# Kernel tuning notes

Measured on AMD Instinct MI355X. Metric: run time of the kernel, lower is better.

Reference implementation:

```python
import jax, jax.numpy as jnp
import numpy as np

N_NODES = 50000
EPS = 1e-5


def sage_conv_max(x, src, dst, W_l, b_l, W_r):
    # PyG SAGEConv(aggr='max'): out = lin_l(max_j x_j) + lin_r(x_i)
    msg = x[src]                                   # [E, d] gather
    agg = jnp.full((x.shape[0], x.shape[1]), -jnp.inf, dtype=x.dtype)
    agg = agg.at[dst].max(msg)                     # scatter-max over edges
    agg = jnp.where(jnp.isneginf(agg), 0.0, agg)   # isolated nodes -> 0 (PyG convention)
    return agg @ W_l.T + b_l + x @ W_r.T


def batch_norm(x, gamma, beta):
    mean = jnp.mean(x, axis=0)
    var = jnp.var(x, axis=0)
    return (x - mean) * jax.lax.rsqrt(var + EPS) * gamma + beta


def setup_inputs() -> dict:
    key = jax.random.key(0)
    ks = jax.random.split(key, 10)
    d_in, d_h, d_out = 128, 128, 32
    s = lambda fan: 1.0 / np.sqrt(fan)
    return {
        "x": jax.random.normal(ks[0], (N_NODES, d_in), dtype=jnp.float32),
        "edge_index": jax.random.randint(ks[1], (2, 800000), 0, N_NODES, dtype=jnp.int32),
        "W_l1": jax.random.uniform(ks[2], (d_h, d_in), jnp.float32, -s(d_in), s(d_in)),
        "b_l1": jnp.zeros((d_h,), jnp.float32),
        "W_r1": jax.random.uniform(ks[3], (d_h, d_in), jnp.float32, -s(d_in), s(d_in)),
        "gamma1": jnp.ones((d_h,), jnp.float32),
        "beta1": jnp.zeros((d_h,), jnp.float32),
        "W_l2": jax.random.uniform(ks[4], (d_out, d_h), jnp.float32, -s(d_h), s(d_h)),
        "b_l2": jnp.zeros((d_out,), jnp.float32),
        "W_r2": jax.random.uniform(ks[5], (d_out, d_h), jnp.float32, -s(d_h), s(d_h)),
    }


def reference(x, edge_index, W_l1, b_l1, W_r1, gamma1, beta1, W_l2, b_l2, W_r2):
    src, dst = edge_index[0], edge_index[1]
    h = sage_conv_max(x, src, dst, W_l1, b_l1, W_r1)
    h = batch_norm(h, gamma1, beta1)
    h = jax.nn.relu(h)
    # dropout is identity at inference
    return sage_conv_max(h, src, dst, W_l2, b_l2, W_r2)
```

## Files before the change

### kernel.cpp

```cpp
#include <hip/hip_runtime.h>
#include <math.h>
#include <float.h>

#define N_NODES 50000
#define N_EDGES 800000
#define NB 392
#define EB 2048
#define NBUCK 196
#define BSH 8
#define CAP 36
#define SEGC 4864
#define CELLS_PER_BUCKET (NB * CAP)
#define FBLK 782

typedef __attribute__((ext_vector_type(8))) short bf16x8;
typedef __attribute__((ext_vector_type(4))) float f32x4;

static __device__ __forceinline__ unsigned short f2bf(float f) {
  unsigned int u = __float_as_uint(f);
  u = (u + 0x7fff + ((u >> 16) & 1)) >> 16;
  return (unsigned short)u;
}

__global__ __launch_bounds__(256) void setup_kernel(
    const int* __restrict__ src, const int* __restrict__ dst,
    unsigned int* __restrict__ pairs, int* __restrict__ counts,
    const float* __restrict__ x, const float* __restrict__ Wl1,
    const float* __restrict__ Wr1, const float* __restrict__ Wl2,
    const float* __restrict__ Wr2, unsigned int* __restrict__ x_bf,
    unsigned short* __restrict__ Wcat1, unsigned short* __restrict__ Wcat2,
    float* __restrict__ gsums) {
  const int b = blockIdx.x, tid = threadIdx.x;
  if (b < NB) {
    __shared__ int cur[NBUCK];
    if (tid < NBUCK) cur[tid] = 0;
    __syncthreads();
#pragma unroll
    for (int it = 0; it < EB / 256; ++it) {
      int e = b * EB + it * 256 + tid;
      if (e < N_EDGES) {
        int d = dst[e];
        int bk = d >> BSH;
        int p = atomicAdd(&cur[bk], 1);
        if (p < CAP)
          pairs[(size_t)(bk * NB + b) * CAP + p] =
              (unsigned)src[e] | ((unsigned)(d & 255) << 16);
      }
    }
    __syncthreads();
    if (tid < NBUCK) {
      int c = cur[tid];
      counts[tid * NB + b] = c > CAP ? CAP : c;
    }
  } else if (b < NB + 6250) {
    int i = (b - NB) * 256 + tid;
    float4 v = ((const float4*)x)[i];
    uint2 o;
    o.x = (unsigned int)f2bf(v.x) | ((unsigned int)f2bf(v.y) << 16);
    o.y = (unsigned int)f2bf(v.z) | ((unsigned int)f2bf(v.w) << 16);
    ((uint2*)x_bf)[i] = o;
  } else if (b < NB + 6410) {
    int i = (b - NB - 6250) * 256 + tid;
    if (i < 32768) {
      int n = i >> 8, k = i & 255;
      float w = (k < 128) ? Wl1[n * 128 + k] : Wr1[n * 128 + (k - 128)];
      Wcat1[i] = f2bf(w);
    } else if (i < 40960) {
      int j = i - 32768;
      int n = j >> 8, k = j & 255;
      float w = (k < 128) ? Wl2[n * 128 + k] : Wr2[n * 128 + (k - 128)];
      Wcat2[j] = f2bf(w);
    }
  } else {
#pragma unroll
    for (int i = 0; i < 8; ++i) gsums[i * 256 + tid] = 0.f;
  }
}

__global__ __launch_bounds__(1024) void bucket_sort(const unsigned int* __restrict__ pairs,
                                                    const int* __restrict__ counts,
                                                    unsigned int* __restrict__ rowinfo,
                                                    int* __restrict__ elist) {
  __shared__ int hist[256], cpos[256], cnt[NB];
  __shared__ int wsum[4];
  const int b = blockIdx.x, tid = threadIdx.x;
  const size_t s0 = (size_t)b * CELLS_PER_BUCKET;
  if (tid < 256) hist[tid] = 0;
  if (tid < NB) cnt[tid] = counts[b * NB + tid];
  __syncthreads();
  for (int p = tid; p < CELLS_PER_BUCKET; p += 1024) {
    int c = p / CAP, s = p - c * CAP;
    if (s < cnt[c]) {
      unsigned int pr = pairs[s0 + p];
      atomicAdd(&hist[(pr >> 16) & 255], 1);
    }
  }
  __syncthreads();
  int incl = 0, h = 0;
  if (tid < 256) {
    const int l = tid & 63;
    h = hist[tid];
    incl = h;
#pragma unroll
    for (int off = 1; off < 64; off <<= 1) {
      int t = __shfl_up(incl, off, 64);
      if (l >= off) incl += t;
    }
    if (l == 63) wsum[tid >> 6] = incl;
  }
  __syncthreads();
  if (tid < 64) {
    int v = (tid < 4) ? wsum[tid] : 0;
#pragma unroll
    for (int off = 1; off < 4; off <<= 1) {
      int t = __shfl_up(v, off, 64);
      if (tid >= off) v += t;
    }
    if (tid < 4) wsum[tid] = v;
  }
  __syncthreads();
  if (tid < 256) {
    const int w = tid >> 6;
    int tot = incl + ((w > 0) ? wsum[w - 1] : 0);
    int excl = tot - h;
    cpos[tid] = excl;
    int node = (b << BSH) + tid;
    if (node < N_NODES)
      rowinfo[node] = (unsigned)(b * SEGC + excl) | ((unsigned)h << 20);
  }
  __syncthreads();
  for (int p = tid; p < CELLS_PER_BUCKET; p += 1024) {
    int c = p / CAP, s = p - c * CAP;
    if (s < cnt[c]) {
      unsigned int pr = pairs[s0 + p];
      int loc = atomicAdd(&cpos[(pr >> 16) & 255], 1);
      elist[b * SEGC + loc] = (int)(pr & 0xffffu);
    }
  }
}

#define ASTR 264

template <int NCOLT, int LDO, bool BF16OUT, bool STATS, bool BN>
__global__ __launch_bounds__(256) void fused_layer(
    const uint4* __restrict__ feat4,
    const unsigned short* __restrict__ Ab,
    const unsigned int* __restrict__ rowinfo,
    const int* __restrict__ elist,
    const unsigned short* __restrict__ Wcat, const float* __restrict__ bias,
    unsigned short* __restrict__ outb, float* __restrict__ outf,
    float* __restrict__ gsums, const float* __restrict__ gamma,
    const float* __restrict__ beta, int N) {
  __shared__ unsigned short Alds[64 * ASTR];
  __shared__ float s_sum[128], s_sq[128];
  __shared__ float s_scale[128], s_shift[128];
  const int tid = threadIdx.x;
  const int rowBase = blockIdx.x * 64;

  if (STATS && tid < 128) { s_sum[tid] = 0.f; s_sq[tid] = 0.f; }
  if (BN) {
    if (tid < 128) {
      float sm = 0.f, sq = 0.f;
#pragma unroll
      for (int r = 0; r < 8; ++r) {
        sm += gsums[r * 256 + tid];
        sq += gsums[r * 256 + 128 + tid];
      }
      const float inv = 1.f / (float)N_NODES;
      float mean = sm * inv;
      float var = sq * inv - mean * mean;
      float sc = gamma[tid] * rsqrtf(var + 1e-5f);
      s_scale[tid] = sc;
      s_shift[tid] = beta[tid] - mean * sc;
    }
    __syncthreads();
  }

#pragma unroll
  for (int it = 0; it < 4; ++it) {
    int f = tid + it * 256;
    int r = f >> 4, seg = f & 15;
    int n = rowBase + r;
    if (n >= N) n = N - 1;
    int4 d = *(const int4*)(Ab + (size_t)n * 128 + seg * 8);
    if (BN) {
      int kb = seg * 8;
      unsigned int* dp = (unsigned int*)&d;
#pragma unroll
      for (int c = 0; c < 4; ++c) {
        int k0 = kb + 2 * c;
        float lo = __uint_as_float(dp[c] << 16);
        float hi = __uint_as_float(dp[c] & 0xffff0000u);
        lo = fmaxf(lo * s_scale[k0] + s_shift[k0], 0.f);
        hi = fmaxf(hi * s_scale[k0 + 1] + s_shift[k0 + 1], 0.f);
        dp[c] = (unsigned)f2bf(lo) | ((unsigned)f2bf(hi) << 16);
      }
    }
    *(int4*)(&Alds[r * ASTR + 128 + seg * 8]) = d;
  }

  const int wv = tid >> 6;
  const int lane = tid & 63;
  const int eslot = lane >> 4;
  const int fq = lane & 15;
  for (int it = 0; it < 16; ++it) {
    int r = wv * 16 + it;
    int node = rowBase + r;
    if (node >= N) node = N - 1;
    unsigned int info = rowinfo[node];
    int e0 = (int)(info & 0xFFFFFu);
    int deg = (int)(info >> 20);
    int e1 = e0 + deg;
    float m[8];
#pragma unroll
    for (int j = 0; j < 8; ++j) m[j] = -FLT_MAX;
    if (deg > 0) {
      const int last = e1 - 1;
      for (int base = e0; base < e1; base += 16) {
        int idx[4];
#pragma unroll
        for (int q = 0; q < 4; ++q) {
          int e = base + q * 4 + eslot;
          if (e > last) e = last;
          idx[q] = elist[e];
        }
        uint4 v[4];
#pragma unroll
        for (int q = 0; q < 4; ++q) v[q] = feat4[(size_t)idx[q] * 16 + fq];
#pragma unroll
        for (int q = 0; q < 4; ++q) {
          const unsigned int* pv = (const unsigned int*)&v[q];
#pragma unroll
          for (int c = 0; c < 4; ++c) {
            m[2 * c]     = fmaxf(m[2 * c],     __uint_as_float(pv[c] << 16));
            m[2 * c + 1] = fmaxf(m[2 * c + 1], __uint_as_float(pv[c] & 0xffff0000u));
          }
        }
      }
    }
#pragma unroll
    for (int j = 0; j < 8; ++j) {
      m[j] = fmaxf(m[j], __shfl_xor(m[j], 16, 64));
      m[j] = fmaxf(m[j], __shfl_xor(m[j], 32, 64));
    }
    if (eslot == 0) {
      if (deg == 0) {
#pragma unroll
        for (int j = 0; j < 8; ++j) m[j] = 0.f;
      } else if (BN) {
#pragma unroll
        for (int j = 0; j < 8; ++j) {
          int col = fq * 8 + j;
          m[j] = fmaxf(m[j] * s_scale[col] + s_shift[col], 0.f);
        }
      }
      int4 o;
      unsigned int* op = (unsigned int*)&o;
      op[0] = (unsigned)f2bf(m[0]) | ((unsigned)f2bf(m[1]) << 16);
      op[1] = (unsigned)f2bf(m[2]) | ((unsigned)f2bf(m[3]) << 16);
      op[2] = (unsigned)f2bf(m[4]) | ((unsigned)f2bf(m[5]) << 16);
      op[3] = (unsigned)f2bf(m[6]) | ((unsigned)f2bf(m[7]) << 16);
      *(int4*)(&Alds[r * ASTR + fq * 8]) = o;
    }
  }

  const int ln15 = lane & 15;
  const int quad = lane >> 4;
  const int ct0 = (NCOLT == 8) ? wv * 2 : 0;
  bf16x8 breg[8][2];
#pragma unroll
  for (int ks = 0; ks < 8; ++ks) {
    const int off = ks * 32 + quad * 8;
#pragma unroll
    for (int j = 0; j < 2; ++j)
      breg[ks][j] = *(const bf16x8*)(Wcat + (size_t)((ct0 + j) * 16 + ln15) * 256 + off);
  }
  __syncthreads();

  float psum[2] = {0.f, 0.f}, psq[2] = {0.f, 0.f};
  const int S0 = (NCOLT == 8) ? 0 : wv;
  const int SN = (NCOLT == 8) ? 4 : 1;
#pragma unroll
  for (int si = 0; si < 4; ++si) {
    if (si >= SN) break;
    const int s = S0 + si;
    const int mrow = s * 16;
    bf16x8 a[8];
#pragma unroll
    for (int ks = 0; ks < 8; ++ks)
      a[ks] = *(const bf16x8*)(&Alds[(mrow + ln15) * ASTR + ks * 32 + quad * 8]);
    f32x4 acc[2] = {};
#pragma unroll
    for (int ks = 0; ks < 8; ++ks)
#pragma unroll
      for (int j = 0; j < 2; ++j)
        acc[j] = __builtin_amdgcn_mfma_f32_16x16x32_bf16(a[ks], breg[ks][j], acc[j], 0, 0, 0);
#pragma unroll
    for (int j = 0; j < 2; ++j) {
      int col = (ct0 + j) * 16 + ln15;
      float bv = bias[col];
#pragma unroll
      for (int i = 0; i < 4; ++i) {
        int r = rowBase + mrow + quad * 4 + i;
        if (r < N) {
          float val = acc[j][i] + bv;
          if (STATS) { psum[j] += val; psq[j] += val * val; }
          if (BF16OUT)
            outb[(size_t)r * LDO + col] = f2bf(val);
          else
            outf[(size_t)r * LDO + col] = val;
        }
      }
    }
  }

  if (STATS) {
#pragma unroll
    for (int j = 0; j < 2; ++j) {
      int col = (ct0 + j) * 16 + ln15;
      atomicAdd(&s_sum[col], psum[j]);
      atomicAdd(&s_sq[col], psq[j]);
    }
    __syncthreads();
    if (tid < 128) {
      int rep = blockIdx.x & 7;
      atomicAdd(&gsums[rep * 256 + tid], s_sum[tid]);
      atomicAdd(&gsums[rep * 256 + 128 + tid], s_sq[tid]);
    }
  }
}

extern "C" void kernel_launch(void* const* d_in, const int* in_sizes, int n_in,
                              void* d_out, int out_size, void* d_ws, size_t ws_size,
                              hipStream_t stream) {
  (void)in_sizes; (void)n_in; (void)out_size; (void)ws_size;
  const float* x     = (const float*)d_in[0];
  const int*   eidx  = (const int*)d_in[1];
  const float* W_l1  = (const float*)d_in[2];
  const float* b_l1  = (const float*)d_in[3];
  const float* W_r1  = (const float*)d_in[4];
  const float* gamma = (const float*)d_in[5];
  const float* beta  = (const float*)d_in[6];
  const float* W_l2  = (const float*)d_in[7];
  const float* b_l2  = (const float*)d_in[8];
  const float* W_r2  = (const float*)d_in[9];
  const int* srcp = eidx;
  const int* dstp = eidx + N_EDGES;
  float* out = (float*)d_out;

  int* wsi = (int*)d_ws;
  float* gsums   = (float*)wsi;
  unsigned int* rowinfo = (unsigned int*)(wsi + 2048);
  int*   counts  = wsi + 52224;
  int*   elist   = wsi + 129056;
  unsigned int* pairs   = (unsigned int*)(wsi + 1082400);
  unsigned int* x_bf    = (unsigned int*)(wsi + 3848352);
  unsigned int* h_bf    = (unsigned int*)(wsi + 10248352);
  unsigned short* Wcat1 = (unsigned short*)(wsi + 13448352);
  unsigned short* Wcat2 = (unsigned short*)(wsi + 13464736);

  setup_kernel<<<dim3(NB + 6410 + 1), 256, 0, stream>>>(
      srcp, dstp, pairs, counts, x, W_l1, W_r1, W_l2, W_r2, x_bf, Wcat1, Wcat2, gsums);

  bucket_sort<<<dim3(NBUCK), 1024, 0, stream>>>(pairs, counts, rowinfo, elist);

  fused_layer<8, 128, true, true, false><<<dim3(FBLK), 256, 0, stream>>>(
      (const uint4*)x_bf, (const unsigned short*)x_bf, rowinfo, elist, Wcat1, b_l1,
      (unsigned short*)h_bf, nullptr, gsums, nullptr, nullptr, N_NODES);

  fused_layer<2, 32, false, false, true><<<dim3(FBLK), 256, 0, stream>>>(
      (const uint4*)h_bf, (const unsigned short*)h_bf, rowinfo, elist, Wcat2, b_l2,
      nullptr, out, gsums, gamma, beta, N_NODES);
}
```

Baseline: 213.9 us.

## Split x bf16 conversion and weight packing across setup and sort kernels

The x-to-bf16 conversion is split in half. The first half stays in the edge-binning kernel, and the second half, the weight concatenation and the gsums zeroing move into extra blocks of the bucket-sort kernel. The bucket sort launches only 196 large blocks and otherwise leaves much of the GPU idle, so the intent is to balance the two launches by filling that idle capacity with independent conversion work. Adding non-sort blocks to the 1024-thread sort kernel could delay scheduling of the sort blocks or raise resource contention.

```diff
diff --git a/kernel.cpp b/kernel.cpp
--- a/kernel.cpp
+++ b/kernel.cpp
@@ -12,6 +12,9 @@
 #define SEGC 4864
 #define CELLS_PER_BUCKET (NB * CAP)
 #define FBLK 782
+#define XH1_BLKS 3125
+#define XH2_BLKS 782
+#define WC_BLKS 40
 
 typedef __attribute__((ext_vector_type(8))) short bf16x8;
 typedef __attribute__((ext_vector_type(4))) float f32x4;
@@ -22,14 +25,10 @@
   return (unsigned short)u;
 }
 
-__global__ __launch_bounds__(256) void setup_kernel(
+__global__ __launch_bounds__(256) void setup_a(
     const int* __restrict__ src, const int* __restrict__ dst,
     unsigned int* __restrict__ pairs, int* __restrict__ counts,
-    const float* __restrict__ x, const float* __restrict__ Wl1,
-    const float* __restrict__ Wr1, const float* __restrict__ Wl2,
-    const float* __restrict__ Wr2, unsigned int* __restrict__ x_bf,
-    unsigned short* __restrict__ Wcat1, unsigned short* __restrict__ Wcat2,
-    float* __restrict__ gsums) {
+    const float* __restrict__ x, unsigned int* __restrict__ x_bf) {
   const int b = blockIdx.x, tid = threadIdx.x;
   if (b < NB) {
     __shared__ int cur[NBUCK];
@@ -52,38 +51,56 @@
       int c = cur[tid];
       counts[tid * NB + b] = c > CAP ? CAP : c;
     }
-  } else if (b < NB + 6250) {
+  } else {
     int i = (b - NB) * 256 + tid;
     float4 v = ((const float4*)x)[i];
     uint2 o;
     o.x = (unsigned int)f2bf(v.x) | ((unsigned int)f2bf(v.y) << 16);
     o.y = (unsigned int)f2bf(v.z) | ((unsigned int)f2bf(v.w) << 16);
     ((uint2*)x_bf)[i] = o;
-  } else if (b < NB + 6410) {
-    int i = (b - NB - 6250) * 256 + tid;
-    if (i < 32768) {
-      int n = i >> 8, k = i & 255;
-      float w = (k < 128) ? Wl1[n * 128 + k] : Wr1[n * 128 + (k - 128)];
-      Wcat1[i] = f2bf(w);
-    } else if (i < 40960) {
-      int j = i - 32768;
-      int n = j >> 8, k = j & 255;
-      float w = (k < 128) ? Wl2[n * 128 + k] : Wr2[n * 128 + (k - 128)];
-      Wcat2[j] = f2bf(w);
-    }
-  } else {
-#pragma unroll
-    for (int i = 0; i < 8; ++i) gsums[i * 256 + tid] = 0.f;
-  }
-}
-
-__global__ __launch_bounds__(1024) void bucket_sort(const unsigned int* __restrict__ pairs,
-                                                    const int* __restrict__ counts,
-                                                    unsigned int* __restrict__ rowinfo,
-                                                    int* __restrict__ elist) {
+  }
+}
+
+__global__ __launch_bounds__(1024) void sort_b(
+    const unsigned int* __restrict__ pairs, const int* __restrict__ counts,
+    unsigned int* __restrict__ rowinfo, int* __restrict__ elist,
+    const float* __restrict__ x, const float* __restrict__ Wl1,
+    const float* __restrict__ Wr1, const float* __restrict__ Wl2,
+    const float* __restrict__ Wr2, unsigned int* __restrict__ x_bf,
+    unsigned short* __restrict__ Wcat1, unsigned short* __restrict__ Wcat2,
+    float* __restrict__ gsums) {
+  const int b = blockIdx.x, tid = threadIdx.x;
+  if (b >= NBUCK) {
+    int bb = b - NBUCK;
+    if (bb < XH2_BLKS) {
+      int i = 800000 + bb * 1024 + tid;
+      if (i < 1600000) {
+        float4 v = ((const float4*)x)[i];
+        uint2 o;
+        o.x = (unsigned int)f2bf(v.x) | ((unsigned int)f2bf(v.y) << 16);
+        o.y = (unsigned int)f2bf(v.z) | ((unsigned int)f2bf(v.w) << 16);
+        ((uint2*)x_bf)[i] = o;
+      }
+    } else if (bb < XH2_BLKS + WC_BLKS) {
+      int i = (bb - XH2_BLKS) * 1024 + tid;
+      if (i < 32768) {
+        int n = i >> 8, k = i & 255;
+        float w = (k < 128) ? Wl1[n * 128 + k] : Wr1[n * 128 + (k - 128)];
+        Wcat1[i] = f2bf(w);
+      } else {
+        int j = i - 32768;
+        int n = j >> 8, k = j & 255;
+        float w = (k < 128) ? Wl2[n * 128 + k] : Wr2[n * 128 + (k - 128)];
+        Wcat2[j] = f2bf(w);
+      }
+    } else {
+      gsums[tid] = 0.f;
+      gsums[tid + 1024] = 0.f;
+    }
+    return;
+  }
   __shared__ int hist[256], cpos[256], cnt[NB];
   __shared__ int wsum[4];
-  const int b = blockIdx.x, tid = threadIdx.x;
   const size_t s0 = (size_t)b * CELLS_PER_BUCKET;
   if (tid < 256) hist[tid] = 0;
   if (tid < NB) cnt[tid] = counts[b * NB + tid];
@@ -359,10 +376,12 @@
   unsigned short* Wcat1 = (unsigned short*)(wsi + 13448352);
   unsigned short* Wcat2 = (unsigned short*)(wsi + 13464736);
 
-  setup_kernel<<<dim3(NB + 6410 + 1), 256, 0, stream>>>(
-      srcp, dstp, pairs, counts, x, W_l1, W_r1, W_l2, W_r2, x_bf, Wcat1, Wcat2, gsums);
-
-  bucket_sort<<<dim3(NBUCK), 1024, 0, stream>>>(pairs, counts, rowinfo, elist);
+  setup_a<<<dim3(NB + XH1_BLKS), 256, 0, stream>>>(
+      srcp, dstp, pairs, counts, x, x_bf);
+
+  sort_b<<<dim3(NBUCK + XH2_BLKS + WC_BLKS + 1), 1024, 0, stream>>>(
+      pairs, counts, rowinfo, elist, x, W_l1, W_r1, W_l2, W_r2,
+      x_bf, Wcat1, Wcat2, gsums);
 
   fused_layer<8, 128, true, true, false><<<dim3(FBLK), 256, 0, stream>>>(
       (const uint4*)x_bf, (const unsigned short*)x_bf, rowinfo, elist, Wcat1, b_l1,
```

Result: no change. 214.7 us (+0.4%).
